# Performance work log

Hardware: AMD Instinct MI355X
Metric: run time of the kernel (lower is better)

The kernel has to match this reference:

```python
import jax, jax.numpy as jnp
import numpy as np

L, B, S, D, H, E, DH, K = 2, 4, 1024, 512, 8, 8, 2048, 2
HEAD = D // H
EPS = 1e-6


def setup_inputs() -> dict:
    key = jax.random.key(0)
    ks = jax.random.split(key, 10)
    s = 0.02
    rn = lambda k, shp: (s * jax.random.normal(k, shp, jnp.float32))
    return {
        "x": jax.random.normal(ks[0], (B, S, D), jnp.float32),
        "ln1_w": jnp.ones((L, D), jnp.float32),
        "ln1_b": jnp.zeros((L, D), jnp.float32),
        "wq": rn(ks[1], (L, D, D)),
        "wk": rn(ks[2], (L, D, D)),
        "wv": rn(ks[3], (L, D, D)),
        "wo": rn(ks[4], (L, D, D)),
        "bo": jnp.zeros((L, D), jnp.float32),
        "ln2_w": jnp.ones((L, D), jnp.float32),
        "ln2_b": jnp.zeros((L, D), jnp.float32),
        "gate_w": rn(ks[5], (L, D, E)),
        "w1": rn(ks[6], (L, E, D, DH)),
        "b1": jnp.zeros((L, E, DH), jnp.float32),
        "w2": rn(ks[7], (L, E, DH, D)),
        "b2": jnp.zeros((L, E, D), jnp.float32),
    }


def _layer_norm(x, w, b):
    mu = jnp.mean(x, axis=-1, keepdims=True)
    var = jnp.mean(jnp.square(x - mu), axis=-1, keepdims=True)
    return (x - mu) * jax.lax.rsqrt(var + EPS) * w + b


def _attention(h, wq_l, wk_l, wv_l, wo_l, bo_l):
    # h: [B,S,D] -> multi-head qk attention (attn_mode='qk'), dropout is eval (identity)
    q = (h @ wq_l).reshape(B, S, H, HEAD)
    k = (h @ wk_l).reshape(B, S, H, HEAD)
    v = (h @ wv_l).reshape(B, S, H, HEAD)
    attn = jnp.einsum('bqhd,bkhd->bhqk', q, k) / np.sqrt(HEAD).astype(np.float32)
    attn = jax.nn.softmax(attn, axis=-1)
    out = jnp.einsum('bhqk,bkhd->bqhd', attn, v).reshape(B, S, D)
    return out @ wo_l + bo_l


def _moe_ffn(x2d, gw, w1_l, b1_l, w2_l, b2_l):
    # x2d: [T,D]; top-k noisy-vmoe gate at eval: clean logits, softmax over the top-k logits
    logits = x2d @ gw  # [T,E]
    topv, topi = jax.lax.top_k(logits, K)  # [T,K]
    gates = jax.nn.softmax(topv, axis=-1)  # [T,K]
    T = x2d.shape[0]
    combine = jnp.zeros((T, E), x2d.dtype).at[jnp.arange(T)[:, None], topi].add(gates)  # [T,E]
    # dense grouped-expert MLP (exact erf GELU as torch.nn.GELU)
    hmid = jax.nn.gelu(jnp.einsum('td,edh->teh', x2d, w1_l) + b1_l[None], approximate=False)
    y = jnp.einsum('teh,ehd->ted', hmid, w2_l) + b2_l[None]
    return jnp.einsum('te,ted->td', combine, y)


def reference(x, ln1_w, ln1_b, wq, wk, wv, wo, bo, ln2_w, ln2_b, gate_w, w1, b1, w2, b2):
    for l in range(L):
        residue = x
        h = _layer_norm(x, ln1_w[l], ln1_b[l])
        x = _attention(h, wq[l], wk[l], wv[l], wo[l], bo[l]) + residue
        residue = x
        h = _layer_norm(x, ln2_w[l], ln2_b[l])
        y = _moe_ffn(h.reshape(B * S, D), gate_w[l], w1[l], b1[l], w2[l], b2[l])
        x = y.reshape(B, S, D) + residue
    return x
```

## Files before the change

### kernel.cpp

```cpp
#include <hip/hip_runtime.h>
#include <cmath>

#define D_MODEL 512
#define T_TOK   4096
#define S_SEQ   1024
#define DH_FF   2048
#define N_EXP   8
#define CAP     9216
#define QKV_LD  1536

typedef __attribute__((ext_vector_type(8))) short bf16x8_t;
typedef __attribute__((ext_vector_type(4))) float f32x4_t;
typedef _Float16 f16x8 __attribute__((ext_vector_type(8)));

__device__ __forceinline__ float gelu_exact(float x) {
    return 0.5f * x * (1.0f + erff(x * 0.70710678118654752440f));
}
__device__ __forceinline__ unsigned short f2bf(float f) {
    union { float f; unsigned int u; } v; v.f = f;
    unsigned int r = v.u + 0x7fff + ((v.u >> 16) & 1);
    return (unsigned short)(r >> 16);
}
__device__ __forceinline__ float bf2f(unsigned short u) {
    union { unsigned int i; float f; } v; v.i = ((unsigned int)u) << 16; return v.f;
}
__device__ __forceinline__ unsigned short f2h(float f) {
    _Float16 h = (_Float16)f;
    return __builtin_bit_cast(unsigned short, h);
}
__device__ __forceinline__ void split1(float v, unsigned short& h, unsigned short& l) {
    _Float16 hf = (_Float16)v;
    _Float16 lf = (_Float16)(v - (float)hf);
    h = __builtin_bit_cast(unsigned short, hf);
    l = __builtin_bit_cast(unsigned short, lf);
}

__global__ __launch_bounds__(256) void ln_kernel(
    const float* __restrict__ x, const float* __restrict__ w,
    const float* __restrict__ b, float* __restrict__ out,
    unsigned short* __restrict__ outb, float* __restrict__ xcopy)
{
    const int t = blockIdx.x, tid = threadIdx.x;
    const float* xr = x + (size_t)t * D_MODEL;
    float v0 = xr[tid], v1 = xr[tid + 256];
    __shared__ float ss[256], sq[256];
    ss[tid] = v0 + v1;
    sq[tid] = v0 * v0 + v1 * v1;
    __syncthreads();
    for (int st = 128; st > 0; st >>= 1) {
        if (tid < st) { ss[tid] += ss[tid + st]; sq[tid] += sq[tid + st]; }
        __syncthreads();
    }
    float mu  = ss[0] * (1.0f / 512.0f);
    float var = sq[0] * (1.0f / 512.0f) - mu * mu;
    float rs  = rsqrtf(var + 1e-6f);
    float o0 = (v0 - mu) * rs * w[tid]       + b[tid];
    float o1 = (v1 - mu) * rs * w[tid + 256] + b[tid + 256];
    float* outr = out + (size_t)t * D_MODEL;
    outr[tid] = o0; outr[tid + 256] = o1;
    if (outb) {
        unsigned short* ob = outb + (size_t)t * D_MODEL;
        ob[tid] = f2bf(o0); ob[tid + 256] = f2bf(o1);
    }
    if (xcopy) {
        float* xc = xcopy + (size_t)t * D_MODEL;
        xc[tid] = v0; xc[tid + 256] = v1;
    }
}

template<int MODE>
__global__ __launch_bounds__(256) void gemm64(
    const float* __restrict__ A, int lda, int KLEN,
    const float* __restrict__ Bw, int ldb, size_t BeStride,
    float* __restrict__ C, int ldc,
    const float* __restrict__ bias, int biasStride,
    const float* __restrict__ resid,
    const int* __restrict__ offs, const int* __restrict__ rowtok, int beta)
{
    __shared__ float Ts[32][68];
    __shared__ unsigned short As_hi[64][40], As_lo[64][40];
    __shared__ unsigned short Bs_hi[64][40], Bs_lo[64][40];
    __shared__ int rt[64];
    __shared__ float rg[64];
    const int tid = threadIdx.x;
    const int row0 = blockIdx.y * 64, col0 = blockIdx.x * 64;
    int e = 0;
    if (MODE == 2 || MODE == 5) {
        #pragma unroll
        for (int i = 1; i < N_EXP; i++) if (offs[i] <= row0) e = i;
        if (tid < 64) rt[tid] = rowtok[row0 + tid];
        if (MODE == 5 && tid >= 64 && tid < 128) rg[tid - 64] = resid[row0 + tid - 64];
        __syncthreads();
    }
    const float* Be = Bw + (size_t)e * BeStride;
    int colB = col0;
    if (MODE == 4) {
        int sel = blockIdx.x >> 3;
        Be = (sel == 0) ? Bw : (sel == 1) ? bias : resid;
        colB = (blockIdx.x & 7) * 64;
    }
    const int lane = tid & 63, w = tid >> 6;
    const int wrow = (w >> 1) * 32, wcol = (w & 1) * 32;
    const int m_ = lane & 15, q_ = lane >> 4;
    f32x4_t acc[2][2];
    #pragma unroll
    for (int i = 0; i < 2; i++)
        #pragma unroll
        for (int j = 0; j < 2; j++) acc[i][j] = (f32x4_t){0.f, 0.f, 0.f, 0.f};

    const int ar = tid >> 2, ac0 = (tid & 3) * 8;
    const int bk = tid >> 3, bn0 = (tid & 7) * 8;
    const int tn = tid & 63, tk4 = (tid >> 6) * 4;

    for (int k0 = 0; k0 < KLEN; k0 += 32) {
        {
            const float* Arow;
            bool zero = false;
            if (MODE == 2) {
                int t = rt[ar];
                zero = (t < 0);
                Arow = A + (size_t)(zero ? 0 : t) * lda;
            } else {
                Arow = A + (size_t)(row0 + ar) * lda;
            }
            #pragma unroll
            for (int q = 0; q < 2; q++) {
                float4 f = zero ? make_float4(0.f, 0.f, 0.f, 0.f)
                                : *(const float4*)&Arow[k0 + ac0 + 4 * q];
                ushort4 h4, l4;
                split1(f.x, h4.x, l4.x); split1(f.y, h4.y, l4.y);
                split1(f.z, h4.z, l4.z); split1(f.w, h4.w, l4.w);
                *(ushort4*)&As_hi[ar][ac0 + 4 * q] = h4;
                *(ushort4*)&As_lo[ar][ac0 + 4 * q] = l4;
            }
        }
        {
            const float* br = &Be[(size_t)(k0 + bk) * ldb + colB + bn0];
            float4 f0 = *(const float4*)&br[0];
            float4 f1 = *(const float4*)&br[4];
            *(float4*)&Ts[bk][bn0]     = f0;
            *(float4*)&Ts[bk][bn0 + 4] = f1;
        }
        __syncthreads();
        #pragma unroll
        for (int rep = 0; rep < 2; rep++) {
            int kk = tk4 + rep * 16;
            ushort4 h4, l4;
            split1(Ts[kk + 0][tn], h4.x, l4.x);
            split1(Ts[kk + 1][tn], h4.y, l4.y);
            split1(Ts[kk + 2][tn], h4.z, l4.z);
            split1(Ts[kk + 3][tn], h4.w, l4.w);
            *(ushort4*)&Bs_hi[tn][kk] = h4;
            *(ushort4*)&Bs_lo[tn][kk] = l4;
        }
        __syncthreads();
        f16x8 ah[2], al[2], bh[2], bl[2];
        #pragma unroll
        for (int i = 0; i < 2; i++) {
            int r = wrow + 16 * i + m_;
            ah[i] = *(const f16x8*)&As_hi[r][q_ * 8];
            al[i] = *(const f16x8*)&As_lo[r][q_ * 8];
        }
        #pragma unroll
        for (int j = 0; j < 2; j++) {
            int r = wcol + 16 * j + m_;
            bh[j] = *(const f16x8*)&Bs_hi[r][q_ * 8];
            bl[j] = *(const f16x8*)&Bs_lo[r][q_ * 8];
        }
        #pragma unroll
        for (int i = 0; i < 2; i++)
            #pragma unroll
            for (int j = 0; j < 2; j++) {
                acc[i][j] = __builtin_amdgcn_mfma_f32_16x16x32_f16(ah[i], bl[j], acc[i][j], 0, 0, 0);
                acc[i][j] = __builtin_amdgcn_mfma_f32_16x16x32_f16(al[i], bh[j], acc[i][j], 0, 0, 0);
                acc[i][j] = __builtin_amdgcn_mfma_f32_16x16x32_f16(ah[i], bh[j], acc[i][j], 0, 0, 0);
            }
        __syncthreads();
    }
    #pragma unroll
    for (int i = 0; i < 2; i++) {
        #pragma unroll
        for (int j = 0; j < 2; j++) {
            #pragma unroll
            for (int r = 0; r < 4; r++) {
                int lr = wrow + 16 * i + q_ * 4 + r;
                int gr = row0 + lr;
                int gc = col0 + wcol + 16 * j + m_;
                float v = acc[i][j][r];
                if (MODE == 5) {
                    int t = rt[lr];
                    if (t >= 0) {
                        float add = beta ? bias[(size_t)e * biasStride + gc] : 0.0f;
                        atomicAdd(&C[(size_t)t * ldc + gc], rg[lr] * (v + add));
                    }
                } else {
                    size_t idx = (size_t)gr * ldc + gc;
                    if (MODE == 1) {
                        C[idx] = v + bias[gc] + resid[idx];
                    } else if (MODE == 2) {
                        C[idx] = gelu_exact(v + bias[(size_t)e * biasStride + gc]);
                    } else {
                        C[idx] = v;
                    }
                }
            }
        }
    }
}

template<int MODE>
__global__ __launch_bounds__(256) void gemm64_bt(
    const unsigned short* __restrict__ A, int lda, int KLEN,
    const float* __restrict__ Bw, int ldb, size_t BeStride,
    unsigned short* __restrict__ C, int ldc,
    const float* __restrict__ biasBase, int biasStride,
    const int* __restrict__ offs, const int* __restrict__ rowtok,
    const float* __restrict__ rowgate, float* __restrict__ Cout, int beta)
{
    __shared__ float Ts[32][68];
    __shared__ unsigned short As[64][40];
    __shared__ unsigned short Bs[64][40];
    __shared__ int rt[64];
    __shared__ float rg[64];
    const int tid = threadIdx.x;
    const int row0 = blockIdx.y * 64, col0 = blockIdx.x * 64;
    int e = 0;
    #pragma unroll
    for (int i = 1; i < N_EXP; i++) if (offs[i] <= row0) e = i;
    if (tid < 64) rt[tid] = rowtok[row0 + tid];
    if (MODE == 5 && tid >= 64 && tid < 128) rg[tid - 64] = rowgate[row0 + tid - 64];
    __syncthreads();
    const float* Be = Bw + (size_t)e * BeStride;
    const int lane = tid & 63, w = tid >> 6;
    const int wrow = (w >> 1) * 32, wcol = (w & 1) * 32;
    const int m_ = lane & 15, q_ = lane >> 4;
    f32x4_t acc[2][2];
    #pragma unroll
    for (int i = 0; i < 2; i++)
        #pragma unroll
        for (int j = 0; j < 2; j++) acc[i][j] = (f32x4_t){0.f, 0.f, 0.f, 0.f};

    const int ar = tid >> 2, ac0 = (tid & 3) * 8;
    const int bk = tid >> 3, bn0 = (tid & 7) * 8;
    const int tn = tid & 63, tk4 = (tid >> 6) * 4;

    for (int k0 = 0; k0 < KLEN; k0 += 32) {
        {
            uint4 val;
            if (MODE == 2) {
                int t = rt[ar];
                val = (t >= 0) ? *(const uint4*)&A[(size_t)t * lda + k0 + ac0]
                               : make_uint4(0u, 0u, 0u, 0u);
            } else {
                val = *(const uint4*)&A[(size_t)(row0 + ar) * lda + k0 + ac0];
            }
            *(uint4*)&As[ar][ac0] = val;
        }
        {
            const float* br = &Be[(size_t)(k0 + bk) * ldb + col0 + bn0];
            float4 f0 = *(const float4*)&br[0];
            float4 f1 = *(const float4*)&br[4];
            *(float4*)&Ts[bk][bn0]     = f0;
            *(float4*)&Ts[bk][bn0 + 4] = f1;
        }
        __syncthreads();
        #pragma unroll
        for (int rep = 0; rep < 2; rep++) {
            int kk = tk4 + rep * 16;
            ushort4 o4;
            o4.x = f2bf(Ts[kk + 0][tn]); o4.y = f2bf(Ts[kk + 1][tn]);
            o4.z = f2bf(Ts[kk + 2][tn]); o4.w = f2bf(Ts[kk + 3][tn]);
            *(ushort4*)&Bs[tn][kk] = o4;
        }
        __syncthreads();
        bf16x8_t af[2], bfr[2];
        #pragma unroll
        for (int i = 0; i < 2; i++)
            af[i] = *(const bf16x8_t*)&As[wrow + 16 * i + m_][q_ * 8];
        #pragma unroll
        for (int j = 0; j < 2; j++)
            bfr[j] = *(const bf16x8_t*)&Bs[wcol + 16 * j + m_][q_ * 8];
        #pragma unroll
        for (int i = 0; i < 2; i++)
            #pragma unroll
            for (int j = 0; j < 2; j++)
                acc[i][j] = __builtin_amdgcn_mfma_f32_16x16x32_bf16(
                    af[i], bfr[j], acc[i][j], 0, 0, 0);
        __syncthreads();
    }
    #pragma unroll
    for (int i = 0; i < 2; i++) {
        #pragma unroll
        for (int j = 0; j < 2; j++) {
            #pragma unroll
            for (int r = 0; r < 4; r++) {
                int lr = wrow + 16 * i + q_ * 4 + r;
                int gr = row0 + lr;
                int gc = col0 + wcol + 16 * j + m_;
                float v = acc[i][j][r];
                if (MODE == 5) {
                    int t = rt[lr];
                    if (t >= 0) {
                        float add = beta ? biasBase[(size_t)e * biasStride + gc] : 0.0f;
                        atomicAdd(&Cout[(size_t)t * ldc + gc], rg[lr] * (v + add));
                    }
                } else {
                    size_t idx = (size_t)gr * ldc + gc;
                    C[idx] = f2bf(gelu_exact(v + biasBase[(size_t)e * biasStride + gc]));
                }
            }
        }
    }
}

__global__ __launch_bounds__(256) void qkv_prep(
    const float* __restrict__ qkvb, unsigned short* __restrict__ Qh,
    unsigned short* __restrict__ Kh, unsigned short* __restrict__ VTh)
{
    __shared__ float Ts[64][65];
    const int tid = threadIdx.x;
    const int t0 = blockIdx.x * 64, hh = blockIdx.y, b = blockIdx.z;
    const int bh = b * 8 + hh;
    const float* src = qkvb + ((size_t)(b * S_SEQ + t0)) * QKV_LD + hh * 64;
    #pragma unroll
    for (int i = 0; i < 4; i++) {
        int flat = tid + i * 256;
        int r = flat >> 4, c4 = (flat & 15) * 4;
        float4 qv = *(const float4*)&src[(size_t)r * QKV_LD + c4];
        float4 kv = *(const float4*)&src[(size_t)r * QKV_LD + 512 + c4];
        float4 vv = *(const float4*)&src[(size_t)r * QKV_LD + 1024 + c4];
        ushort4 qo, ko;
        qo.x = f2h(qv.x * 0.125f); qo.y = f2h(qv.y * 0.125f);
        qo.z = f2h(qv.z * 0.125f); qo.w = f2h(qv.w * 0.125f);
        ko.x = f2h(kv.x); ko.y = f2h(kv.y); ko.z = f2h(kv.z); ko.w = f2h(kv.w);
        size_t o = ((size_t)bh * S_SEQ + t0 + r) * 64 + c4;
        *(ushort4*)&Qh[o] = qo;
        *(ushort4*)&Kh[o] = ko;
        Ts[r][c4] = vv.x; Ts[r][c4 + 1] = vv.y; Ts[r][c4 + 2] = vv.z; Ts[r][c4 + 3] = vv.w;
    }
    __syncthreads();
    #pragma unroll
    for (int i = 0; i < 4; i++) {
        int flat = tid + i * 256;
        int d = flat >> 4, s4 = (flat & 15) * 4;
        ushort4 vo;
        vo.x = f2h(Ts[s4][d]);     vo.y = f2h(Ts[s4 + 1][d]);
        vo.z = f2h(Ts[s4 + 2][d]); vo.w = f2h(Ts[s4 + 3][d]);
        *(ushort4*)&VTh[((size_t)bh * 64 + d) * S_SEQ + t0 + s4] = vo;
    }
}

__global__ __launch_bounds__(256) void flash_attn_mfma(
    const unsigned short* __restrict__ Qh, const unsigned short* __restrict__ Kh,
    const unsigned short* __restrict__ VTh, float* __restrict__ out)
{
    __shared__ unsigned short Ks[64 * 72];
    __shared__ unsigned short Vt[64 * 72];
    __shared__ unsigned short Ps[64 * 72];
    const int tid = threadIdx.x;
    const int lane = tid & 63, w = tid >> 6;
    const int m_ = lane & 15, q_ = lane >> 4;
    const int hh = blockIdx.y, b = blockIdx.z;
    const int bh = b * 8 + hh;
    const int q0 = blockIdx.x * 64;
    const size_t qbase = ((size_t)bh * S_SEQ + q0) * 64;
    const size_t kbase = (size_t)bh * S_SEQ * 64;
    const size_t vbase = (size_t)bh * 64 * S_SEQ;

    f16x8 qa[2];
    #pragma unroll
    for (int c = 0; c < 2; c++)
        qa[c] = *(const f16x8*)&Qh[qbase + (size_t)(w * 16 + m_) * 64 + c * 32 + q_ * 8];

    float m_run[4], l_run[4];
    f32x4_t acc[4];
    #pragma unroll
    for (int r = 0; r < 4; r++) { m_run[r] = -INFINITY; l_run[r] = 0.0f; }
    #pragma unroll
    for (int oj = 0; oj < 4; oj++) acc[oj] = (f32x4_t){0.f, 0.f, 0.f, 0.f};

    for (int kv0 = 0; kv0 < S_SEQ; kv0 += 64) {
        __syncthreads();
        #pragma unroll
        for (int i = 0; i < 2; i++) {
            int g = tid + i * 256;
            int r = g >> 3, c8 = (g & 7) * 8;
            *(uint4*)&Ks[r * 72 + c8] =
                *(const uint4*)&Kh[kbase + (size_t)(kv0 + r) * 64 + c8];
            *(uint4*)&Vt[r * 72 + c8] =
                *(const uint4*)&VTh[vbase + (size_t)r * S_SEQ + kv0 + c8];
        }
        __syncthreads();
        f32x4_t s[4];
        #pragma unroll
        for (int j = 0; j < 4; j++) s[j] = (f32x4_t){0.f, 0.f, 0.f, 0.f};
        #pragma unroll
        for (int c = 0; c < 2; c++)
            #pragma unroll
            for (int j = 0; j < 4; j++) {
                f16x8 kb = *(const f16x8*)&Ks[(j * 16 + m_) * 72 + c * 32 + q_ * 8];
                s[j] = __builtin_amdgcn_mfma_f32_16x16x32_f16(qa[c], kb, s[j], 0, 0, 0);
            }
        float alpha[4];
        #pragma unroll
        for (int r = 0; r < 4; r++) {
            float rm = fmaxf(fmaxf(s[0][r], s[1][r]), fmaxf(s[2][r], s[3][r]));
            #pragma unroll
            for (int mk = 1; mk < 16; mk <<= 1)
                rm = fmaxf(rm, __shfl_xor(rm, mk));
            float mn = fmaxf(m_run[r], rm);
            alpha[r] = __expf(m_run[r] - mn);
            m_run[r] = mn;
            float ps = 0.0f;
            #pragma unroll
            for (int j = 0; j < 4; j++) {
                float p = __expf(s[j][r] - mn);
                s[j][r] = p;
                ps += p;
            }
            #pragma unroll
            for (int mk = 1; mk < 16; mk <<= 1)
                ps += __shfl_xor(ps, mk);
            l_run[r] = l_run[r] * alpha[r] + ps;
        }
        #pragma unroll
        for (int oj = 0; oj < 4; oj++)
            #pragma unroll
            for (int r = 0; r < 4; r++)
                acc[oj][r] *= alpha[r];
        #pragma unroll
        for (int j = 0; j < 4; j++)
            #pragma unroll
            for (int r = 0; r < 4; r++)
                Ps[(w * 16 + q_ * 4 + r) * 72 + j * 16 + m_] = f2h(s[j][r]);
        __syncthreads();
        #pragma unroll
        for (int c = 0; c < 2; c++) {
            f16x8 pa = *(const f16x8*)&Ps[(w * 16 + m_) * 72 + c * 32 + q_ * 8];
            #pragma unroll
            for (int oj = 0; oj < 4; oj++) {
                f16x8 vb = *(const f16x8*)&Vt[(oj * 16 + m_) * 72 + c * 32 + q_ * 8];
                acc[oj] = __builtin_amdgcn_mfma_f32_16x16x32_f16(pa, vb, acc[oj], 0, 0, 0);
            }
        }
    }
    const size_t obase = ((size_t)b * S_SEQ + q0) * D_MODEL + hh * 64;
    #pragma unroll
    for (int r = 0; r < 4; r++) {
        float inv = 1.0f / l_run[r];
        #pragma unroll
        for (int oj = 0; oj < 4; oj++)
            out[obase + (size_t)(w * 16 + q_ * 4 + r) * D_MODEL + oj * 16 + m_] =
                acc[oj][r] * inv;
    }
}

__global__ __launch_bounds__(256) void gate_kernel(
    const float* __restrict__ h, const float* __restrict__ gw,
    int* __restrict__ topi, float* __restrict__ gates)
{
    const int w = threadIdx.x >> 6, lane = threadIdx.x & 63;
    const int t = blockIdx.x * 4 + w;
    const float* hr = h + (size_t)t * D_MODEL;
    float acc[N_EXP] = {};
    for (int d = lane; d < D_MODEL; d += 64) {
        float xv = hr[d];
        const float4 g0 = *(const float4*)&gw[(size_t)d * N_EXP];
        const float4 g1 = *(const float4*)&gw[(size_t)d * N_EXP + 4];
        acc[0] += xv * g0.x; acc[1] += xv * g0.y;
        acc[2] += xv * g0.z; acc[3] += xv * g0.w;
        acc[4] += xv * g1.x; acc[5] += xv * g1.y;
        acc[6] += xv * g1.z; acc[7] += xv * g1.w;
    }
    #pragma unroll
    for (int mk = 1; mk < 64; mk <<= 1) {
        #pragma unroll
        for (int e = 0; e < N_EXP; e++) acc[e] += __shfl_xor(acc[e], mk);
    }
    if (lane == 0) {
        int e0 = 0; float v0 = acc[0];
        #pragma unroll
        for (int e = 1; e < N_EXP; e++) if (acc[e] > v0) { v0 = acc[e]; e0 = e; }
        int e1 = -1; float v1 = -INFINITY;
        #pragma unroll
        for (int e = 0; e < N_EXP; e++) if (e != e0 && acc[e] > v1) { v1 = acc[e]; e1 = e; }
        float g0 = 1.0f / (1.0f + __expf(v1 - v0));
        float g1 = 1.0f - g0;
        topi[2 * t] = e0; topi[2 * t + 1] = e1;
        gates[2 * t] = g0; gates[2 * t + 1] = g1;
    }
}

__global__ __launch_bounds__(1024) void route_kernel(
    const int* __restrict__ topi, const float* __restrict__ gates,
    int* __restrict__ offs, int* __restrict__ rowtok, float* __restrict__ rowgate)
{
    __shared__ int wcnt[16][N_EXP];
    __shared__ int wbase[16][N_EXP];
    __shared__ int offs_s[N_EXP + 1];
    const int tid = threadIdx.x, w = tid >> 6, lane = tid & 63;
    const unsigned long long lt = (1ULL << lane) - 1ULL;

    int mye[8];
    int cnt[N_EXP] = {};
    #pragma unroll
    for (int r = 0; r < 8; r++) {
        int i = w * 512 + r * 64 + lane;
        int e = topi[i];
        mye[r] = e;
        #pragma unroll
        for (int e8 = 0; e8 < N_EXP; e8++) {
            unsigned long long m = __ballot(e == e8);
            cnt[e8] += (int)__popcll(m);
        }
    }
    if (lane == 0) {
        #pragma unroll
        for (int e8 = 0; e8 < N_EXP; e8++) wcnt[w][e8] = cnt[e8];
    }
    __syncthreads();
    if (tid == 0) {
        int off = 0;
        for (int e8 = 0; e8 < N_EXP; e8++) {
            offs_s[e8] = off;
            int c = 0;
            for (int ww = 0; ww < 16; ww++) c += wcnt[ww][e8];
            off += (c + 127) & ~127;
        }
        offs_s[N_EXP] = off;
        for (int e8 = 0; e8 <= N_EXP; e8++) offs[e8] = offs_s[e8];
    }
    __syncthreads();
    if (tid < 128) {
        int ww = tid >> 3, e8 = tid & 7;
        int bse = offs_s[e8];
        for (int w2 = 0; w2 < ww; w2++) bse += wcnt[w2][e8];
        wbase[ww][e8] = bse;
    }
    __syncthreads();
    int base[N_EXP];
    #pragma unroll
    for (int e8 = 0; e8 < N_EXP; e8++) base[e8] = wbase[w][e8];
    #pragma unroll
    for (int r = 0; r < 8; r++) {
        int i = w * 512 + r * 64 + lane;
        int e = mye[r];
        int pos = 0;
        #pragma unroll
        for (int e8 = 0; e8 < N_EXP; e8++) {
            unsigned long long m = __ballot(e == e8);
            if (e == e8) pos = base[e8] + (int)__popcll(m & lt);
            base[e8] += (int)__popcll(m);
        }
        rowtok[pos] = i >> 1;
        rowgate[pos] = gates[i];
    }
}

extern "C" void kernel_launch(void* const* d_in, const int* in_sizes, int n_in,
                              void* d_out, int out_size, void* d_ws, size_t ws_size,
                              hipStream_t stream)
{
    const float* x0    = (const float*)d_in[0];
    const float* ln1w  = (const float*)d_in[1];
    const float* ln1b  = (const float*)d_in[2];
    const float* wq    = (const float*)d_in[3];
    const float* wk    = (const float*)d_in[4];
    const float* wv    = (const float*)d_in[5];
    const float* wo    = (const float*)d_in[6];
    const float* bo    = (const float*)d_in[7];
    const float* ln2w  = (const float*)d_in[8];
    const float* ln2b  = (const float*)d_in[9];
    const float* gatew = (const float*)d_in[10];
    const float* w1    = (const float*)d_in[11];
    const float* b1    = (const float*)d_in[12];
    const float* w2    = (const float*)d_in[13];
    const float* b2    = (const float*)d_in[14];
    float* out = (float*)d_out;

    char* ws = (char*)d_ws;
    const size_t MiB = 1 << 20;
    float* x1   = (float*)(ws + 0);
    float* h    = (float*)(ws + 8 * MiB);
    float* attn = (float*)(ws + 8 * MiB);
    float* h2   = (float*)(ws + 8 * MiB);
    float* qkvb = (float*)(ws + 16 * MiB);
    unsigned short* Qh  = (unsigned short*)(ws + 0);
    unsigned short* Kh  = (unsigned short*)(ws + 4 * MiB);
    unsigned short* VTh = (unsigned short*)(ws + 40 * MiB);
    float* hmid_f32 = (float*)(ws + 16 * MiB);
    unsigned short* hmid_bf16 = (unsigned short*)(ws + 16 * MiB);
    unsigned short* h2b       = (unsigned short*)(ws + 43 * MiB);
    size_t oI = 47 * MiB;
    int*   topi    = (int*)(ws + oI);
    float* gates   = (float*)(ws + oI + 2 * T_TOK * 4);
    int*   rowtok  = (int*)(ws + oI + 4 * T_TOK * 4);
    float* rowgate = (float*)(ws + oI + 4 * T_TOK * 4 + CAP * 4);
    int*   meta    = (int*)(ws + oI + 4 * T_TOK * 4 + 2 * CAP * 4);
    int* offs = meta;
    float* x2 = out;

    const dim3 gQKV(24, T_TOK / 64);
    const dim3 gO(D_MODEL / 64, T_TOK / 64);
    const dim3 gUp1(8, CAP / 64);
    const dim3 gDn1(D_MODEL / 64, CAP / 64);
    const dim3 gUp2(16, CAP / 64);
    const dim3 gDn2(D_MODEL / 64, CAP / 64);
    const dim3 gAttn(S_SEQ / 64, 8, 4);

    for (int l = 0; l < 2; l++) {
        const float* xin = (l == 0) ? x0 : x2;
        float* xout = (l == 1) ? out : x2;
        const float* wq_l = wq + (size_t)l * D_MODEL * D_MODEL;
        const float* wk_l = wk + (size_t)l * D_MODEL * D_MODEL;
        const float* wv_l = wv + (size_t)l * D_MODEL * D_MODEL;
        const float* wo_l = wo + (size_t)l * D_MODEL * D_MODEL;
        const float* w1_l = w1 + (size_t)l * N_EXP * D_MODEL * DH_FF;
        const float* w2_l = w2 + (size_t)l * N_EXP * DH_FF * D_MODEL;
        const float* b1_l = b1 + (size_t)l * N_EXP * DH_FF;
        const float* b2_l = b2 + (size_t)l * N_EXP * D_MODEL;

        ln_kernel<<<T_TOK, 256, 0, stream>>>(xin, ln1w + (size_t)l * D_MODEL,
                                             ln1b + (size_t)l * D_MODEL, h,
                                             nullptr, nullptr);
        gemm64<4><<<gQKV, 256, 0, stream>>>(h, D_MODEL, D_MODEL, wq_l, D_MODEL, 0,
                                            qkvb, QKV_LD, wk_l, 0, wv_l,
                                            nullptr, nullptr, 0);
        qkv_prep<<<gAttn, 256, 0, stream>>>(qkvb, Qh, Kh, VTh);
        flash_attn_mfma<<<gAttn, 256, 0, stream>>>(Qh, Kh, VTh, attn);
        gemm64<1><<<gO, 256, 0, stream>>>(attn, D_MODEL, D_MODEL, wo_l, D_MODEL, 0,
                                          x1, D_MODEL, bo + (size_t)l * D_MODEL, 0,
                                          xin, nullptr, nullptr, 0);
        ln_kernel<<<T_TOK, 256, 0, stream>>>(x1, ln2w + (size_t)l * D_MODEL,
                                             ln2b + (size_t)l * D_MODEL, h2,
                                             (l == 1) ? h2b : nullptr, xout);

        hipMemsetAsync(rowtok, 0xFF, CAP * 4, stream);
        gate_kernel<<<T_TOK / 4, 256, 0, stream>>>(h2, gatew + (size_t)l * D_MODEL * N_EXP,
                                                   topi, gates);
        route_kernel<<<1, 1024, 0, stream>>>(topi, gates, offs, rowtok, rowgate);

        if (l == 0) {
            for (int c = 0; c < 4; c++) {
                gemm64<2><<<gUp1, 256, 0, stream>>>(h2, D_MODEL, D_MODEL,
                                                    w1_l + (size_t)c * 512, DH_FF,
                                                    (size_t)D_MODEL * DH_FF,
                                                    hmid_f32, 512,
                                                    b1_l + (size_t)c * 512, DH_FF,
                                                    nullptr, offs, rowtok, 0);
                gemm64<5><<<gDn1, 256, 0, stream>>>(hmid_f32, 512, 512,
                                                    w2_l + (size_t)c * 512 * D_MODEL,
                                                    D_MODEL, (size_t)DH_FF * D_MODEL,
                                                    xout, D_MODEL, b2_l, D_MODEL,
                                                    rowgate, offs, rowtok,
                                                    (c == 0) ? 1 : 0);
            }
        } else {
            for (int c = 0; c < 2; c++) {
                gemm64_bt<2><<<gUp2, 256, 0, stream>>>(h2b, D_MODEL, D_MODEL,
                                                       w1_l + (size_t)c * 1024, DH_FF,
                                                       (size_t)D_MODEL * DH_FF,
                                                       hmid_bf16, 1024,
                                                       b1_l + (size_t)c * 1024, DH_FF,
                                                       offs, rowtok, nullptr, nullptr, 0);
                gemm64_bt<5><<<gDn2, 256, 0, stream>>>(hmid_bf16, 1024, 1024,
                                                       w2_l + (size_t)c * 1024 * D_MODEL,
                                                       D_MODEL, (size_t)DH_FF * D_MODEL,
                                                       nullptr, D_MODEL, b2_l, D_MODEL,
                                                       offs, rowtok, rowgate, xout,
                                                       (c == 0) ? 1 : 0);
            }
        }
    }
}
```

Before: 948.0 us.

## Pre-transpose and pre-split weights and activations before GEMMs

Weights are now transposed and split into fp16 hi/lo (or converted to bf16) by separate small kernels before each GEMM. Producers (layernorm, flash attention, the up-projection epilogue) write activations directly as hi/lo halves. This removes the per-tile fp32 load, shared-memory transpose and split work, and one barrier, from the GEMM inner loops. The bf16 GEMM also moves to a K=64 step. The cost is extra launches and extra global traffic for the converted copies, which are redone on every call.

```diff
diff --git a/kernel.cpp b/kernel.cpp
--- a/kernel.cpp
+++ b/kernel.cpp
@@ -37,7 +37,8 @@
 
 __global__ __launch_bounds__(256) void ln_kernel(
     const float* __restrict__ x, const float* __restrict__ w,
-    const float* __restrict__ b, float* __restrict__ out,
+    const float* __restrict__ b, float* __restrict__ outf,
+    unsigned short* __restrict__ outHi, unsigned short* __restrict__ outLo,
     unsigned short* __restrict__ outb, float* __restrict__ xcopy)
 {
     const int t = blockIdx.x, tid = threadIdx.x;
@@ -56,8 +57,18 @@
     float rs  = rsqrtf(var + 1e-6f);
     float o0 = (v0 - mu) * rs * w[tid]       + b[tid];
     float o1 = (v1 - mu) * rs * w[tid + 256] + b[tid + 256];
-    float* outr = out + (size_t)t * D_MODEL;
-    outr[tid] = o0; outr[tid + 256] = o1;
+    if (outf) {
+        float* outr = outf + (size_t)t * D_MODEL;
+        outr[tid] = o0; outr[tid + 256] = o1;
+    }
+    if (outHi) {
+        unsigned short h0, l0, h1, l1;
+        split1(o0, h0, l0); split1(o1, h1, l1);
+        unsigned short* oh = outHi + (size_t)t * D_MODEL;
+        unsigned short* ol = outLo + (size_t)t * D_MODEL;
+        oh[tid] = h0; oh[tid + 256] = h1;
+        ol[tid] = l0; ol[tid + 256] = l1;
+    }
     if (outb) {
         unsigned short* ob = outb + (size_t)t * D_MODEL;
         ob[tid] = f2bf(o0); ob[tid + 256] = f2bf(o1);
@@ -68,16 +79,62 @@
     }
 }
 
+__global__ __launch_bounds__(256) void tconv_split(
+    const float* __restrict__ in, int inLd, size_t eStrideIn,
+    unsigned short* __restrict__ outHi, unsigned short* __restrict__ outLo,
+    int outLd, size_t eStrideOut)
+{
+    __shared__ float Ts[32][33];
+    const int tid = threadIdx.x;
+    const int k0 = blockIdx.y * 32, n0 = blockIdx.x * 32;
+    in    += (size_t)blockIdx.z * eStrideIn;
+    outHi += (size_t)blockIdx.z * eStrideOut;
+    outLo += (size_t)blockIdx.z * eStrideOut;
+    int r = tid >> 3, c = (tid & 7) * 4;
+    float4 v = *(const float4*)&in[(size_t)(k0 + r) * inLd + n0 + c];
+    Ts[r][c] = v.x; Ts[r][c + 1] = v.y; Ts[r][c + 2] = v.z; Ts[r][c + 3] = v.w;
+    __syncthreads();
+    int n = tid >> 3, kk = (tid & 7) * 4;
+    ushort4 h4, l4;
+    split1(Ts[kk][n],     h4.x, l4.x); split1(Ts[kk + 1][n], h4.y, l4.y);
+    split1(Ts[kk + 2][n], h4.z, l4.z); split1(Ts[kk + 3][n], h4.w, l4.w);
+    size_t o = (size_t)(n0 + n) * outLd + k0 + kk;
+    *(ushort4*)&outHi[o] = h4;
+    *(ushort4*)&outLo[o] = l4;
+}
+
+__global__ __launch_bounds__(256) void tconv(
+    const float* __restrict__ in, int inLd, size_t eStrideIn,
+    unsigned short* __restrict__ out, int outLd, size_t eStrideOut)
+{
+    __shared__ float Ts[32][33];
+    const int tid = threadIdx.x;
+    const int k0 = blockIdx.y * 32, n0 = blockIdx.x * 32;
+    in  += (size_t)blockIdx.z * eStrideIn;
+    out += (size_t)blockIdx.z * eStrideOut;
+    int r = tid >> 3, c = (tid & 7) * 4;
+    float4 v = *(const float4*)&in[(size_t)(k0 + r) * inLd + n0 + c];
+    Ts[r][c] = v.x; Ts[r][c + 1] = v.y; Ts[r][c + 2] = v.z; Ts[r][c + 3] = v.w;
+    __syncthreads();
+    int n = tid >> 3, kk = (tid & 7) * 4;
+    ushort4 o;
+    o.x = f2bf(Ts[kk][n]);     o.y = f2bf(Ts[kk + 1][n]);
+    o.z = f2bf(Ts[kk + 2][n]); o.w = f2bf(Ts[kk + 3][n]);
+    *(ushort4*)&out[(size_t)(n0 + n) * outLd + k0 + kk] = o;
+}
+
 template<int MODE>
-__global__ __launch_bounds__(256) void gemm64(
-    const float* __restrict__ A, int lda, int KLEN,
-    const float* __restrict__ Bw, int ldb, size_t BeStride,
+__global__ __launch_bounds__(256) void gemm_pre(
+    const unsigned short* __restrict__ Ahi, const unsigned short* __restrict__ Alo,
+    int lda, int KLEN,
+    const unsigned short* __restrict__ Bhi, const unsigned short* __restrict__ Blo,
+    size_t BeStride,
     float* __restrict__ C, int ldc,
     const float* __restrict__ bias, int biasStride,
     const float* __restrict__ resid,
-    const int* __restrict__ offs, const int* __restrict__ rowtok, int beta)
-{
-    __shared__ float Ts[32][68];
+    const int* __restrict__ offs, const int* __restrict__ rowtok, int beta,
+    unsigned short* __restrict__ Chi, unsigned short* __restrict__ Clo)
+{
     __shared__ unsigned short As_hi[64][40], As_lo[64][40];
     __shared__ unsigned short Bs_hi[64][40], Bs_lo[64][40];
     __shared__ int rt[64];
@@ -92,13 +149,8 @@
         if (MODE == 5 && tid >= 64 && tid < 128) rg[tid - 64] = resid[row0 + tid - 64];
         __syncthreads();
     }
-    const float* Be = Bw + (size_t)e * BeStride;
-    int colB = col0;
-    if (MODE == 4) {
-        int sel = blockIdx.x >> 3;
-        Be = (sel == 0) ? Bw : (sel == 1) ? bias : resid;
-        colB = (blockIdx.x & 7) * 64;
-    }
+    const unsigned short* BeH = Bhi + (size_t)e * BeStride;
+    const unsigned short* BeL = Blo + (size_t)e * BeStride;
     const int lane = tid & 63, w = tid >> 6;
     const int wrow = (w >> 1) * 32, wcol = (w & 1) * 32;
     const int m_ = lane & 15, q_ = lane >> 4;
@@ -108,51 +160,25 @@
         #pragma unroll
         for (int j = 0; j < 2; j++) acc[i][j] = (f32x4_t){0.f, 0.f, 0.f, 0.f};
 
-    const int ar = tid >> 2, ac0 = (tid & 3) * 8;
-    const int bk = tid >> 3, bn0 = (tid & 7) * 8;
-    const int tn = tid & 63, tk4 = (tid >> 6) * 4;
+    const int sr = tid >> 2, sc = (tid & 3) * 8;
+    size_t arow;
+    bool azero = false;
+    if (MODE == 2) {
+        int t = rt[sr];
+        azero = (t < 0);
+        arow = (size_t)(azero ? 0 : t) * lda;
+    } else {
+        arow = (size_t)(row0 + sr) * lda;
+    }
+    const size_t brow = (size_t)(col0 + sr) * KLEN;
 
     for (int k0 = 0; k0 < KLEN; k0 += 32) {
-        {
-            const float* Arow;
-            bool zero = false;
-            if (MODE == 2) {
-                int t = rt[ar];
-                zero = (t < 0);
-                Arow = A + (size_t)(zero ? 0 : t) * lda;
-            } else {
-                Arow = A + (size_t)(row0 + ar) * lda;
-            }
-            #pragma unroll
-            for (int q = 0; q < 2; q++) {
-                float4 f = zero ? make_float4(0.f, 0.f, 0.f, 0.f)
-                                : *(const float4*)&Arow[k0 + ac0 + 4 * q];
-                ushort4 h4, l4;
-                split1(f.x, h4.x, l4.x); split1(f.y, h4.y, l4.y);
-                split1(f.z, h4.z, l4.z); split1(f.w, h4.w, l4.w);
-                *(ushort4*)&As_hi[ar][ac0 + 4 * q] = h4;
-                *(ushort4*)&As_lo[ar][ac0 + 4 * q] = l4;
-            }
-        }
-        {
-            const float* br = &Be[(size_t)(k0 + bk) * ldb + colB + bn0];
-            float4 f0 = *(const float4*)&br[0];
-            float4 f1 = *(const float4*)&br[4];
-            *(float4*)&Ts[bk][bn0]     = f0;
-            *(float4*)&Ts[bk][bn0 + 4] = f1;
-        }
-        __syncthreads();
-        #pragma unroll
-        for (int rep = 0; rep < 2; rep++) {
-            int kk = tk4 + rep * 16;
-            ushort4 h4, l4;
-            split1(Ts[kk + 0][tn], h4.x, l4.x);
-            split1(Ts[kk + 1][tn], h4.y, l4.y);
-            split1(Ts[kk + 2][tn], h4.z, l4.z);
-            split1(Ts[kk + 3][tn], h4.w, l4.w);
-            *(ushort4*)&Bs_hi[tn][kk] = h4;
-            *(ushort4*)&Bs_lo[tn][kk] = l4;
-        }
+        uint4 vh = azero ? make_uint4(0u, 0u, 0u, 0u) : *(const uint4*)&Ahi[arow + k0 + sc];
+        uint4 vl = azero ? make_uint4(0u, 0u, 0u, 0u) : *(const uint4*)&Alo[arow + k0 + sc];
+        *(uint4*)&As_hi[sr][sc] = vh;
+        *(uint4*)&As_lo[sr][sc] = vl;
+        *(uint4*)&Bs_hi[sr][sc] = *(const uint4*)&BeH[brow + k0 + sc];
+        *(uint4*)&Bs_lo[sr][sc] = *(const uint4*)&BeL[brow + k0 + sc];
         __syncthreads();
         f16x8 ah[2], al[2], bh[2], bl[2];
         #pragma unroll
@@ -193,15 +219,16 @@
                         float add = beta ? bias[(size_t)e * biasStride + gc] : 0.0f;
                         atomicAdd(&C[(size_t)t * ldc + gc], rg[lr] * (v + add));
                     }
+                } else if (MODE == 2) {
+                    float g = gelu_exact(v + bias[(size_t)e * biasStride + gc]);
+                    unsigned short gh, gl;
+                    split1(g, gh, gl);
+                    size_t idx = (size_t)gr * ldc + gc;
+                    Chi[idx] = gh; Clo[idx] = gl;
                 } else {
                     size_t idx = (size_t)gr * ldc + gc;
-                    if (MODE == 1) {
-                        C[idx] = v + bias[gc] + resid[idx];
-                    } else if (MODE == 2) {
-                        C[idx] = gelu_exact(v + bias[(size_t)e * biasStride + gc]);
-                    } else {
-                        C[idx] = v;
-                    }
+                    if (MODE == 1) C[idx] = v + bias[gc] + resid[idx];
+                    else           C[idx] = v;
                 }
             }
         }
@@ -209,17 +236,16 @@
 }
 
 template<int MODE>
-__global__ __launch_bounds__(256) void gemm64_bt(
+__global__ __launch_bounds__(256) void gemm_pre_bt(
     const unsigned short* __restrict__ A, int lda, int KLEN,
-    const float* __restrict__ Bw, int ldb, size_t BeStride,
+    const unsigned short* __restrict__ Bt, size_t BeStride,
     unsigned short* __restrict__ C, int ldc,
     const float* __restrict__ biasBase, int biasStride,
     const int* __restrict__ offs, const int* __restrict__ rowtok,
     const float* __restrict__ rowgate, float* __restrict__ Cout, int beta)
 {
-    __shared__ float Ts[32][68];
-    __shared__ unsigned short As[64][40];
-    __shared__ unsigned short Bs[64][40];
+    __shared__ unsigned short As[64][72];
+    __shared__ unsigned short Bs[64][72];
     __shared__ int rt[64];
     __shared__ float rg[64];
     const int tid = threadIdx.x;
@@ -230,7 +256,7 @@
     if (tid < 64) rt[tid] = rowtok[row0 + tid];
     if (MODE == 5 && tid >= 64 && tid < 128) rg[tid - 64] = rowgate[row0 + tid - 64];
     __syncthreads();
-    const float* Be = Bw + (size_t)e * BeStride;
+    const unsigned short* Be = Bt + (size_t)e * BeStride;
     const int lane = tid & 63, w = tid >> 6;
     const int wrow = (w >> 1) * 32, wcol = (w & 1) * 32;
     const int m_ = lane & 15, q_ = lane >> 4;
@@ -240,52 +266,48 @@
         #pragma unroll
         for (int j = 0; j < 2; j++) acc[i][j] = (f32x4_t){0.f, 0.f, 0.f, 0.f};
 
-    const int ar = tid >> 2, ac0 = (tid & 3) * 8;
-    const int bk = tid >> 3, bn0 = (tid & 7) * 8;
-    const int tn = tid & 63, tk4 = (tid >> 6) * 4;
-
-    for (int k0 = 0; k0 < KLEN; k0 += 32) {
-        {
-            uint4 val;
-            if (MODE == 2) {
-                int t = rt[ar];
-                val = (t >= 0) ? *(const uint4*)&A[(size_t)t * lda + k0 + ac0]
-                               : make_uint4(0u, 0u, 0u, 0u);
-            } else {
-                val = *(const uint4*)&A[(size_t)(row0 + ar) * lda + k0 + ac0];
-            }
-            *(uint4*)&As[ar][ac0] = val;
-        }
-        {
-            const float* br = &Be[(size_t)(k0 + bk) * ldb + col0 + bn0];
-            float4 f0 = *(const float4*)&br[0];
-            float4 f1 = *(const float4*)&br[4];
-            *(float4*)&Ts[bk][bn0]     = f0;
-            *(float4*)&Ts[bk][bn0 + 4] = f1;
-        }
-        __syncthreads();
-        #pragma unroll
-        for (int rep = 0; rep < 2; rep++) {
-            int kk = tk4 + rep * 16;
-            ushort4 o4;
-            o4.x = f2bf(Ts[kk + 0][tn]); o4.y = f2bf(Ts[kk + 1][tn]);
-            o4.z = f2bf(Ts[kk + 2][tn]); o4.w = f2bf(Ts[kk + 3][tn]);
-            *(ushort4*)&Bs[tn][kk] = o4;
-        }
-        __syncthreads();
-        bf16x8_t af[2], bfr[2];
-        #pragma unroll
-        for (int i = 0; i < 2; i++)
-            af[i] = *(const bf16x8_t*)&As[wrow + 16 * i + m_][q_ * 8];
-        #pragma unroll
-        for (int j = 0; j < 2; j++)
-            bfr[j] = *(const bf16x8_t*)&Bs[wcol + 16 * j + m_][q_ * 8];
-        #pragma unroll
-        for (int i = 0; i < 2; i++)
+    const int sr = tid >> 3, sc = (tid & 7) * 8;
+    size_t arow0, arow1;
+    bool az0 = false, az1 = false;
+    {
+        int r1 = sr + 32;
+        if (MODE == 2) {
+            int t0 = rt[sr], t1 = rt[r1];
+            az0 = (t0 < 0); az1 = (t1 < 0);
+            arow0 = (size_t)(az0 ? 0 : t0) * lda;
+            arow1 = (size_t)(az1 ? 0 : t1) * lda;
+        } else {
+            arow0 = (size_t)(row0 + sr) * lda;
+            arow1 = (size_t)(row0 + r1) * lda;
+        }
+    }
+    const size_t brow0 = (size_t)(col0 + sr) * KLEN;
+    const size_t brow1 = (size_t)(col0 + sr + 32) * KLEN;
+
+    for (int k0 = 0; k0 < KLEN; k0 += 64) {
+        uint4 a0 = az0 ? make_uint4(0u, 0u, 0u, 0u) : *(const uint4*)&A[arow0 + k0 + sc];
+        uint4 a1 = az1 ? make_uint4(0u, 0u, 0u, 0u) : *(const uint4*)&A[arow1 + k0 + sc];
+        *(uint4*)&As[sr][sc]      = a0;
+        *(uint4*)&As[sr + 32][sc] = a1;
+        *(uint4*)&Bs[sr][sc]      = *(const uint4*)&Be[brow0 + k0 + sc];
+        *(uint4*)&Bs[sr + 32][sc] = *(const uint4*)&Be[brow1 + k0 + sc];
+        __syncthreads();
+        #pragma unroll
+        for (int ks = 0; ks < 2; ks++) {
+            bf16x8_t af[2], bfr[2];
+            #pragma unroll
+            for (int i = 0; i < 2; i++)
+                af[i] = *(const bf16x8_t*)&As[wrow + 16 * i + m_][ks * 32 + q_ * 8];
             #pragma unroll
             for (int j = 0; j < 2; j++)
-                acc[i][j] = __builtin_amdgcn_mfma_f32_16x16x32_bf16(
-                    af[i], bfr[j], acc[i][j], 0, 0, 0);
+                bfr[j] = *(const bf16x8_t*)&Bs[wcol + 16 * j + m_][ks * 32 + q_ * 8];
+            #pragma unroll
+            for (int i = 0; i < 2; i++)
+                #pragma unroll
+                for (int j = 0; j < 2; j++)
+                    acc[i][j] = __builtin_amdgcn_mfma_f32_16x16x32_bf16(
+                        af[i], bfr[j], acc[i][j], 0, 0, 0);
+        }
         __syncthreads();
     }
     #pragma unroll
@@ -305,8 +327,8 @@
                         atomicAdd(&Cout[(size_t)t * ldc + gc], rg[lr] * (v + add));
                     }
                 } else {
-                    size_t idx = (size_t)gr * ldc + gc;
-                    C[idx] = f2bf(gelu_exact(v + biasBase[(size_t)e * biasStride + gc]));
+                    C[(size_t)gr * ldc + gc] =
+                        f2bf(gelu_exact(v + biasBase[(size_t)e * biasStride + gc]));
                 }
             }
         }
@@ -352,7 +374,8 @@
 
 __global__ __launch_bounds__(256) void flash_attn_mfma(
     const unsigned short* __restrict__ Qh, const unsigned short* __restrict__ Kh,
-    const unsigned short* __restrict__ VTh, float* __restrict__ out)
+    const unsigned short* __restrict__ VTh,
+    unsigned short* __restrict__ outHi, unsigned short* __restrict__ outLo)
 {
     __shared__ unsigned short Ks[64 * 72];
     __shared__ unsigned short Vt[64 * 72];
@@ -449,9 +472,14 @@
     for (int r = 0; r < 4; r++) {
         float inv = 1.0f / l_run[r];
         #pragma unroll
-        for (int oj = 0; oj < 4; oj++)
-            out[obase + (size_t)(w * 16 + q_ * 4 + r) * D_MODEL + oj * 16 + m_] =
-                acc[oj][r] * inv;
+        for (int oj = 0; oj < 4; oj++) {
+            float v = acc[oj][r] * inv;
+            unsigned short vh, vl;
+            split1(v, vh, vl);
+            size_t idx = obase + (size_t)(w * 16 + q_ * 4 + r) * D_MODEL + oj * 16 + m_;
+            outHi[idx] = vh;
+            outLo[idx] = vl;
+        }
     }
 }
 
@@ -580,27 +608,44 @@
 
     char* ws = (char*)d_ws;
     const size_t MiB = 1 << 20;
-    float* x1   = (float*)(ws + 0);
-    float* h    = (float*)(ws + 8 * MiB);
-    float* attn = (float*)(ws + 8 * MiB);
-    float* h2   = (float*)(ws + 8 * MiB);
+    unsigned short* Qh    = (unsigned short*)(ws + 0);
+    unsigned short* Kh    = (unsigned short*)(ws + 4 * MiB);
+    unsigned short* h_hi  = (unsigned short*)(ws + 8 * MiB);
+    unsigned short* h_lo  = (unsigned short*)(ws + 12 * MiB);
+    unsigned short* attn_hi = (unsigned short*)(ws + 8 * MiB);
+    unsigned short* attn_lo = (unsigned short*)(ws + 12 * MiB);
     float* qkvb = (float*)(ws + 16 * MiB);
-    unsigned short* Qh  = (unsigned short*)(ws + 0);
-    unsigned short* Kh  = (unsigned short*)(ws + 4 * MiB);
-    unsigned short* VTh = (unsigned short*)(ws + 40 * MiB);
-    float* hmid_f32 = (float*)(ws + 16 * MiB);
-    unsigned short* hmid_bf16 = (unsigned short*)(ws + 16 * MiB);
-    unsigned short* h2b       = (unsigned short*)(ws + 43 * MiB);
-    size_t oI = 47 * MiB;
+    float* x1   = (float*)(ws + 16 * MiB);
+    unsigned short* wqkvT_hi = (unsigned short*)(ws + 40 * MiB);
+    unsigned short* wqkvT_lo = (unsigned short*)(ws + 40 * MiB + QKV_LD * D_MODEL * 2);
+    unsigned short* VTh   = (unsigned short*)(ws + 40 * MiB);
+    unsigned short* woT_hi = (unsigned short*)(ws + 44 * MiB);
+    unsigned short* woT_lo = (unsigned short*)(ws + 44 * MiB + D_MODEL * D_MODEL * 2);
+    unsigned short* h2_hi = (unsigned short*)(ws + 0);
+    unsigned short* h2_lo = (unsigned short*)(ws + 4 * MiB);
+    unsigned short* h2b   = (unsigned short*)(ws + 0);
+    float* h2 = (float*)(ws + 8 * MiB);
+    unsigned short* w1T_hi = (unsigned short*)(ws + 8 * MiB);
+    unsigned short* w1T_lo = (unsigned short*)(ws + 12 * MiB);
+    unsigned short* w2T_hi = (unsigned short*)(ws + 16 * MiB);
+    unsigned short* w2T_lo = (unsigned short*)(ws + 20 * MiB);
+    unsigned short* hmid_hi = (unsigned short*)(ws + 24 * MiB);
+    unsigned short* hmid_lo = (unsigned short*)(ws + 33 * MiB);
+    unsigned short* w1T_bf  = (unsigned short*)(ws + 8 * MiB);
+    unsigned short* w2T_bf  = (unsigned short*)(ws + 16 * MiB);
+    unsigned short* hmidb   = (unsigned short*)(ws + 24 * MiB);
+    size_t oI = 46 * MiB;
     int*   topi    = (int*)(ws + oI);
     float* gates   = (float*)(ws + oI + 2 * T_TOK * 4);
     int*   rowtok  = (int*)(ws + oI + 4 * T_TOK * 4);
     float* rowgate = (float*)(ws + oI + 4 * T_TOK * 4 + CAP * 4);
-    int*   meta    = (int*)(ws + oI + 4 * T_TOK * 4 + 2 * CAP * 4);
-    int* offs = meta;
+    int*   offs    = (int*)(ws + oI + 4 * T_TOK * 4 + 2 * CAP * 4);
     float* x2 = out;
 
-    const dim3 gQKV(24, T_TOK / 64);
+    const dim3 gW(16, 16, 1);
+    const dim3 gW8(16, 16, 8);
+    const dim3 gW8b(16, 32, 8);
+    const dim3 gQKV(QKV_LD / 64, T_TOK / 64);
     const dim3 gO(D_MODEL / 64, T_TOK / 64);
     const dim3 gUp1(8, CAP / 64);
     const dim3 gDn1(D_MODEL / 64, CAP / 64);
@@ -621,18 +666,30 @@
         const float* b2_l = b2 + (size_t)l * N_EXP * D_MODEL;
 
         ln_kernel<<<T_TOK, 256, 0, stream>>>(xin, ln1w + (size_t)l * D_MODEL,
-                                             ln1b + (size_t)l * D_MODEL, h,
-                                             nullptr, nullptr);
-        gemm64<4><<<gQKV, 256, 0, stream>>>(h, D_MODEL, D_MODEL, wq_l, D_MODEL, 0,
-                                            qkvb, QKV_LD, wk_l, 0, wv_l,
-                                            nullptr, nullptr, 0);
+                                             ln1b + (size_t)l * D_MODEL,
+                                             nullptr, h_hi, h_lo, nullptr, nullptr);
+        tconv_split<<<gW, 256, 0, stream>>>(wq_l, D_MODEL, 0, wqkvT_hi, wqkvT_lo, D_MODEL, 0);
+        tconv_split<<<gW, 256, 0, stream>>>(wk_l, D_MODEL, 0,
+                                            wqkvT_hi + 512 * 512, wqkvT_lo + 512 * 512,
+                                            D_MODEL, 0);
+        tconv_split<<<gW, 256, 0, stream>>>(wv_l, D_MODEL, 0,
+                                            wqkvT_hi + 1024 * 512, wqkvT_lo + 1024 * 512,
+                                            D_MODEL, 0);
+        tconv_split<<<gW, 256, 0, stream>>>(wo_l, D_MODEL, 0, woT_hi, woT_lo, D_MODEL, 0);
+        gemm_pre<0><<<gQKV, 256, 0, stream>>>(h_hi, h_lo, D_MODEL, D_MODEL,
+                                              wqkvT_hi, wqkvT_lo, 0,
+                                              qkvb, QKV_LD, nullptr, 0, nullptr,
+                                              nullptr, nullptr, 0, nullptr, nullptr);
         qkv_prep<<<gAttn, 256, 0, stream>>>(qkvb, Qh, Kh, VTh);
-        flash_attn_mfma<<<gAttn, 256, 0, stream>>>(Qh, Kh, VTh, attn);
-        gemm64<1><<<gO, 256, 0, stream>>>(attn, D_MODEL, D_MODEL, wo_l, D_MODEL, 0,
-                                          x1, D_MODEL, bo + (size_t)l * D_MODEL, 0,
-                                          xin, nullptr, nullptr, 0);
+        flash_attn_mfma<<<gAttn, 256, 0, stream>>>(Qh, Kh, VTh, attn_hi, attn_lo);
+        gemm_pre<1><<<gO, 256, 0, stream>>>(attn_hi, attn_lo, D_MODEL, D_MODEL,
+                                            woT_hi, woT_lo, 0,
+                                            x1, D_MODEL, bo + (size_t)l * D_MODEL, 0,
+                                            xin, nullptr, nullptr, 0, nullptr, nullptr);
         ln_kernel<<<T_TOK, 256, 0, stream>>>(x1, ln2w + (size_t)l * D_MODEL,
                                              ln2b + (size_t)l * D_MODEL, h2,
+                                             (l == 0) ? h2_hi : nullptr,
+                                             (l == 0) ? h2_lo : nullptr,
                                              (l == 1) ? h2b : nullptr, xout);
 
         hipMemsetAsync(rowtok, 0xFF, CAP * 4, stream);
@@ -642,33 +699,44 @@
 
         if (l == 0) {
             for (int c = 0; c < 4; c++) {
-                gemm64<2><<<gUp1, 256, 0, stream>>>(h2, D_MODEL, D_MODEL,
-                                                    w1_l + (size_t)c * 512, DH_FF,
-                                                    (size_t)D_MODEL * DH_FF,
-                                                    hmid_f32, 512,
-                                                    b1_l + (size_t)c * 512, DH_FF,
-                                                    nullptr, offs, rowtok, 0);
-                gemm64<5><<<gDn1, 256, 0, stream>>>(hmid_f32, 512, 512,
-                                                    w2_l + (size_t)c * 512 * D_MODEL,
-                                                    D_MODEL, (size_t)DH_FF * D_MODEL,
-                                                    xout, D_MODEL, b2_l, D_MODEL,
-                                                    rowgate, offs, rowtok,
-                                                    (c == 0) ? 1 : 0);
+                tconv_split<<<gW8, 256, 0, stream>>>(w1_l + (size_t)c * 512, DH_FF,
+                                                     (size_t)D_MODEL * DH_FF,
+                                                     w1T_hi, w1T_lo, D_MODEL,
+                                                     (size_t)512 * D_MODEL);
+                gemm_pre<2><<<gUp1, 256, 0, stream>>>(h2_hi, h2_lo, D_MODEL, D_MODEL,
+                                                      w1T_hi, w1T_lo, (size_t)512 * D_MODEL,
+                                                      nullptr, 512,
+                                                      b1_l + (size_t)c * 512, DH_FF,
+                                                      nullptr, offs, rowtok, 0,
+                                                      hmid_hi, hmid_lo);
+                tconv_split<<<gW8, 256, 0, stream>>>(w2_l + (size_t)c * 512 * D_MODEL,
+                                                     D_MODEL, (size_t)DH_FF * D_MODEL,
+                                                     w2T_hi, w2T_lo, 512,
+                                                     (size_t)D_MODEL * 512);
+                gemm_pre<5><<<gDn1, 256, 0, stream>>>(hmid_hi, hmid_lo, 512, 512,
+                                                      w2T_hi, w2T_lo, (size_t)D_MODEL * 512,
+                                                      xout, D_MODEL, b2_l, D_MODEL,
+                                                      rowgate, offs, rowtok,
+                                                      (c == 0) ? 1 : 0, nullptr, nullptr);
             }
         } else {
             for (int c = 0; c < 2; c++) {
-                gemm64_bt<2><<<gUp2, 256, 0, stream>>>(h2b, D_MODEL, D_MODEL,
-                                                       w1_l + (size_t)c * 1024, DH_FF,
-                                                       (size_t)D_MODEL * DH_FF,
-                                                       hmid_bf16, 1024,
-                                                       b1_l + (size_t)c * 1024, DH_FF,
-                                                       offs, rowtok, nullptr, nullptr, 0);
-                gemm64_bt<5><<<gDn2, 256, 0, stream>>>(hmid_bf16, 1024, 1024,
-                                                       w2_l + (size_t)c * 1024 * D_MODEL,
-                                                       D_MODEL, (size_t)DH_FF * D_MODEL,
-                                                       nullptr, D_MODEL, b2_l, D_MODEL,
-                                                       offs, rowtok, rowgate, xout,
-                                                       (c == 0) ? 1 : 0);
+                tconv<<<dim3(32, 16, 8), 256, 0, stream>>>(
+                    w1_l + (size_t)c * 1024, DH_FF, (size_t)D_MODEL * DH_FF,
+                    w1T_bf, D_MODEL, (size_t)1024 * D_MODEL);
+                gemm_pre_bt<2><<<gUp2, 256, 0, stream>>>(h2b, D_MODEL, D_MODEL,
+                                                         w1T_bf, (size_t)1024 * D_MODEL,
+                                                         hmidb, 1024,
+                                                         b1_l + (size_t)c * 1024, DH_FF,
+                                                         offs, rowtok, nullptr, nullptr, 0);
+                tconv<<<dim3(16, 32, 8), 256, 0, stream>>>(
+                    w2_l + (size_t)c * 1024 * D_MODEL, D_MODEL, (size_t)DH_FF * D_MODEL,
+                    w2T_bf, 1024, (size_t)D_MODEL * 1024);
+                gemm_pre_bt<5><<<gDn2, 256, 0, stream>>>(hmidb, 1024, 1024,
+                                                         w2T_bf, (size_t)D_MODEL * 1024,
+                                                         nullptr, D_MODEL, b2_l, D_MODEL,
+                                                         offs, rowtok, rowgate, xout,
+                                                         (c == 0) ? 1 : 0);
             }
         }
     }
```

Result: faster. 922.1 us (-2.7%).
